# Kernel tuning notes

Hardware: AMD Instinct MI355X
Metric: run time of the kernel (lower is better)

## Reference

```python
import jax, jax.numpy as jnp
import numpy as np

B, NX, C, KX = 16, 8192, 128, 16  # batch, grid size, channels, retained positive modes


def setup_inputs() -> dict:
    key = jax.random.key(0)
    k1, k2, k3 = jax.random.split(key, 3)
    x = jax.random.normal(k1, (B, NX, C), dtype=jnp.float32)
    scale = 1.0 / (C ** 2)
    w_real = scale * jax.random.uniform(k2, (KX + 1, C, C), dtype=jnp.float32)
    w_imag = scale * jax.random.uniform(k3, (KX + 1, C, C), dtype=jnp.float32)
    return {"x": x, "w_real": w_real, "w_imag": w_imag}


def reference(x, w_real, w_imag):
    # x: (b, nx, c); weights: (kx+1, c, c) complex
    nx = x.shape[1]
    k1 = w_real.shape[0]  # kx + 1 retained frequencies
    w = w_real + 1j * w_imag
    fx = jnp.fft.rfft(x, axis=-2)  # (b, nx//2+1, c) complex
    # torch.matmul(weights, fx[:, :kx+1, :, None])[..., 0]:
    # out[b,k,i] = sum_j w[k,i,j] * fx[b,k,j]
    out_ft = jnp.einsum('kij,bkj->bki', w, fx[:, :k1, :])
    # zero-pad truncated spectrum back to full rfft length, then inverse
    pad = nx // 2 + 1 - k1
    out_full = jnp.pad(out_ft, ((0, 0), (0, pad), (0, 0)))
    return jnp.fft.irfft(out_full, n=nx, axis=-2)
```

## Files before the change

kernel.cpp:

```cpp
#include <hip/hip_runtime.h>
#include <math.h>

#define B_     16
#define NX_    8192
#define C_     128
#define K1_    17
#define NC_    64
#define NH_    4096

typedef float v2f __attribute__((ext_vector_type(2)));

#define GPART_F ((size_t)B_ * K1_ * 2 * NC_ * C_)

__global__ __launch_bounds__(256) void k_fwd(const float* __restrict__ x,
                                             float* __restrict__ ws) {
    __shared__ float smem[8960];

    float* gpart = ws;
    const int b = blockIdx.y;
    const int c = blockIdx.x;
    const int t = threadIdx.x;
    const int j2 = t & 63;
    const int h = t >> 6;
    const int i0 = c * 64;

    {
        float2* tg = (float2*)smem;
        for (int idx = t; idx < 64 * K1_; idx += 256) {
            int i = idx / K1_;
            int k = idx - i * K1_;
            int m = (k * (i0 + i)) & (NX_ - 1);
            float rev = (float)m * (1.0f / (float)NX_);
            tg[idx] = make_float2(__builtin_amdgcn_cosf(rev),
                                  __builtin_amdgcn_sinf(rev));
        }
    }
    __syncthreads();

    v2f gr[K1_], gs[K1_];
#pragma unroll
    for (int k = 0; k < K1_; ++k) { gr[k] = (v2f)(0.f); gs[k] = (v2f)(0.f); }

    const size_t xb = (size_t)b * NX_ * C_;
    const float2* tl = (const float2*)smem + (size_t)h * 16 * K1_;
#pragma unroll 4
    for (int s = 0; s < 16; ++s) {
        const int i = h * 16 + s;
        const int nlo = i0 + i;
        v2f xlo = *(const v2f*)(x + xb + (size_t)nlo * C_ + 2 * j2);
        v2f xhi = (v2f)(0.f);
        if (nlo > 0)
            xhi = *(const v2f*)(x + xb + (size_t)(NX_ - nlo) * C_ + 2 * j2);
        v2f xp = xlo + xhi;
        v2f xm = xlo - xhi;
        const float2* tr = tl + s * K1_;
#pragma unroll
        for (int k = 0; k < K1_; ++k) {
            float2 tt = tr[k];
            v2f cc = {tt.x, tt.x};
            v2f ss = {tt.y, tt.y};
            gr[k] = __builtin_elementwise_fma(xp, cc, gr[k]);
            gs[k] = __builtin_elementwise_fma(xm, ss, gs[k]);
        }
    }

    float2* red = (float2*)smem;
    __syncthreads();
    if (h >= 2) {
        float2* p = red + ((h - 2) * 64 + j2) * 35;
#pragma unroll
        for (int k = 0; k < K1_; ++k) {
            p[2 * k]     = make_float2(gr[k].x, gr[k].y);
            p[2 * k + 1] = make_float2(gs[k].x, gs[k].y);
        }
    }
    __syncthreads();
    if (h < 2) {
        const float2* p = red + (h * 64 + j2) * 35;
#pragma unroll
        for (int k = 0; k < K1_; ++k) {
            float2 a = p[2 * k], cc = p[2 * k + 1];
            gr[k].x += a.x;  gr[k].y += a.y;
            gs[k].x += cc.x; gs[k].y += cc.y;
        }
    }
    __syncthreads();
    if (h == 1) {
        float2* p = red + j2 * 35;
#pragma unroll
        for (int k = 0; k < K1_; ++k) {
            p[2 * k]     = make_float2(gr[k].x, gr[k].y);
            p[2 * k + 1] = make_float2(gs[k].x, gs[k].y);
        }
    }
    __syncthreads();
    if (h == 0) {
        const float2* p = red + j2 * 35;
        v2f x4 = (v2f)(0.f);
        if (c == 0)
            x4 = *(const v2f*)(x + xb + (size_t)NH_ * C_ + 2 * j2);
#pragma unroll
        for (int k = 0; k < K1_; ++k) {
            float2 a = p[2 * k], cc = p[2 * k + 1];
            gr[k].x += a.x;  gr[k].y += a.y;
            gs[k].x += cc.x; gs[k].y += cc.y;
            gr[k] += (k & 1) ? -x4 : x4;
            float* gpR = gpart + ((((size_t)b * K1_ + k) * 2 + 0) * NC_ + c) * C_;
            float* gpS = gpart + ((((size_t)b * K1_ + k) * 2 + 1) * NC_ + c) * C_;
            ((v2f*)gpR)[j2] = gr[k];
            ((v2f*)gpS)[j2] = gs[k];
        }
    }
}

__global__ __launch_bounds__(256) void k_mix(const float* __restrict__ wr_g,
                                             const float* __restrict__ wi_g,
                                             float* __restrict__ ws) {
    const int k = blockIdx.x;
    const int b = blockIdx.y;
    const int t = threadIdx.x;
    const int i = t & 127;
    const int h = t >> 7;

    const float* gpart = ws;
    float2* acoef = (float2*)(ws + GPART_F);

    __shared__ float grs[C_], gss[C_], tr_[C_], ti_[C_];

    const float* baseR = gpart + (((size_t)b * K1_ + k) * 2 + 0) * ((size_t)NC_ * C_);
    const float* baseS = gpart + (((size_t)b * K1_ + k) * 2 + 1) * ((size_t)NC_ * C_);
    float gr = 0.f, gs = 0.f;
#pragma unroll
    for (int s = 0; s < 32; ++s) {
        gr += baseR[(size_t)(h * 32 + s) * C_ + i];
        gs += baseS[(size_t)(h * 32 + s) * C_ + i];
    }
    if (h) { tr_[i] = gr; ti_[i] = gs; }
    __syncthreads();
    if (!h) { grs[i] = gr + tr_[i]; gss[i] = gs + ti_[i]; }
    __syncthreads();

    float hr = 0.f, hi = 0.f;
    const float* wrp = wr_g + ((size_t)k * C_ + i) * C_;
    const float* wip = wi_g + ((size_t)k * C_ + i) * C_;
#pragma unroll 8
    for (int jj = h * 64; jj < h * 64 + 64; ++jj) {
        float wr = wrp[jj], wi = wip[jj];
        float a = grs[jj], cc = gss[jj];
        hr = fmaf(wr, a, hr); hr = fmaf( wi, cc, hr);
        hi = fmaf(wi, a, hi); hi = fmaf(-wr, cc, hi);
    }
    __syncthreads();
    if (h) { tr_[i] = hr; ti_[i] = hi; }
    __syncthreads();
    if (!h) {
        hr += tr_[i]; hi += ti_[i];
        float cf = (k == 0 ? 1.0f : 2.0f) / (float)NX_;
        acoef[((size_t)b * K1_ + k) * C_ + i] = make_float2(cf * hr, -cf * hi);
    }
}

__global__ __launch_bounds__(256) void k_inv(float* __restrict__ out,
                                             const float* __restrict__ ws) {
    __shared__ float2 smem[64 * K1_];

    const float4* acoef4 = (const float4*)(ws + GPART_F);
    const int b = blockIdx.y;
    const int c = blockIdx.x;
    const int t = threadIdx.x;
    const int jp = t & 63;
    const int h = t >> 6;
    const int i0 = c * 64;

    for (int idx = t; idx < 64 * K1_; idx += 256) {
        int i = idx / K1_;
        int k = idx - i * K1_;
        int m = (k * (i0 + i)) & (NX_ - 1);
        float rev = (float)m * (1.0f / (float)NX_);
        smem[idx] = make_float2(__builtin_amdgcn_cosf(rev),
                                __builtin_amdgcn_sinf(rev));
    }

    v2f arP[K1_], aiP[K1_];
#pragma unroll
    for (int k = 0; k < K1_; ++k) {
        float4 a = acoef4[((size_t)b * K1_ + k) * (C_ / 2) + jp];
        arP[k] = (v2f){a.x, a.z};
        aiP[k] = (v2f){a.y, a.w};
    }
    __syncthreads();

    const size_t ob = (size_t)b * NX_ * C_;
    const float2* tl = smem + (size_t)h * 16 * K1_;
#pragma unroll 4
    for (int s = 0; s < 16; ++s) {
        const int nlo = i0 + h * 16 + s;
        const float2* tr = tl + s * K1_;
        v2f S1 = (v2f)(0.f), S2 = (v2f)(0.f);
#pragma unroll
        for (int k = 0; k < K1_; ++k) {
            float2 tt = tr[k];
            v2f cc = {tt.x, tt.x};
            v2f ss = {tt.y, tt.y};
            S1 = __builtin_elementwise_fma(arP[k], cc, S1);
            S2 = __builtin_elementwise_fma(aiP[k], ss, S2);
        }
        *(v2f*)(out + ob + (size_t)nlo * C_ + 2 * jp) = S1 + S2;
        if (nlo > 0)
            *(v2f*)(out + ob + (size_t)(NX_ - nlo) * C_ + 2 * jp) = S1 - S2;
    }

    if (c == 0 && h == 0) {
        v2f o = (v2f)(0.f);
#pragma unroll
        for (int k = 0; k < K1_; ++k) o += (k & 1) ? -arP[k] : arP[k];
        *(v2f*)(out + ob + (size_t)NH_ * C_ + 2 * jp) = o;
    }
}

extern "C" void kernel_launch(void* const* d_in, const int* in_sizes, int n_in,
                              void* d_out, int out_size, void* d_ws, size_t ws_size,
                              hipStream_t stream) {
    const float* x  = (const float*)d_in[0];
    const float* wr = (const float*)d_in[1];
    const float* wi = (const float*)d_in[2];
    float* out = (float*)d_out;
    float* ws  = (float*)d_ws;

    k_fwd<<<dim3(NC_, B_), 256, 0, stream>>>(x, ws);
    k_mix<<<dim3(K1_, B_), 256, 0, stream>>>(wr, wi, ws);
    k_inv<<<dim3(NC_, B_), 256, 0, stream>>>(out, ws);
}
```

Baseline: 53.63 us.

## Split forward DFT frequencies across half-waves with float4 loads; widen mix kernel

The forward kernel now has each thread load four channels as a float4 and handle half of the retained frequencies, 9 of 18 padded. This halves per-thread accumulator count and doubles the work done per memory load, and the Nyquist correction moves before the reduction. The mix kernel moves from 256 to 1024 threads per block, splitting both the partial-sum reduction and the weight contraction into more, shorter pieces for more parallelism. Costs are an extra padded frequency slot and more shared-memory reduction traffic.

```diff
diff --git a/kernel.cpp b/kernel.cpp
--- a/kernel.cpp
+++ b/kernel.cpp
@@ -5,156 +5,172 @@
 #define NX_    8192
 #define C_     128
 #define K1_    17
+#define KP_    18
 #define NC_    64
 #define NH_    4096
 
 typedef float v2f __attribute__((ext_vector_type(2)));
+typedef float v4f __attribute__((ext_vector_type(4)));
 
 #define GPART_F ((size_t)B_ * K1_ * 2 * NC_ * C_)
 
 __global__ __launch_bounds__(256) void k_fwd(const float* __restrict__ x,
                                              float* __restrict__ ws) {
-    __shared__ float smem[8960];
+    __shared__ v4f smem[2 * 64 * 19];
 
     float* gpart = ws;
     const int b = blockIdx.y;
     const int c = blockIdx.x;
     const int t = threadIdx.x;
-    const int j2 = t & 63;
-    const int h = t >> 6;
-    const int i0 = c * 64;
+    const int jq  = t & 31;
+    const int sub = (t >> 5) & 1;
+    const int w   = t >> 6;
+    const int i0  = c * 64;
 
     {
         float2* tg = (float2*)smem;
-        for (int idx = t; idx < 64 * K1_; idx += 256) {
-            int i = idx / K1_;
-            int k = idx - i * K1_;
-            int m = (k * (i0 + i)) & (NX_ - 1);
-            float rev = (float)m * (1.0f / (float)NX_);
-            tg[idx] = make_float2(__builtin_amdgcn_cosf(rev),
-                                  __builtin_amdgcn_sinf(rev));
-        }
-    }
-    __syncthreads();
-
-    v2f gr[K1_], gs[K1_];
-#pragma unroll
-    for (int k = 0; k < K1_; ++k) { gr[k] = (v2f)(0.f); gs[k] = (v2f)(0.f); }
+        for (int idx = t; idx < 64 * KP_; idx += 256) {
+            int i = idx / KP_;
+            int k = idx - i * KP_;
+            float2 v = make_float2(0.f, 0.f);
+            if (k < K1_) {
+                int m = (k * (i0 + i)) & (NX_ - 1);
+                float rev = (float)m * (1.0f / (float)NX_);
+                v = make_float2(__builtin_amdgcn_cosf(rev),
+                                __builtin_amdgcn_sinf(rev));
+            }
+            tg[idx] = v;
+        }
+    }
+    __syncthreads();
+
+    v4f gr[9], gs[9];
+#pragma unroll
+    for (int kk = 0; kk < 9; ++kk) { gr[kk] = (v4f)(0.f); gs[kk] = (v4f)(0.f); }
 
     const size_t xb = (size_t)b * NX_ * C_;
-    const float2* tl = (const float2*)smem + (size_t)h * 16 * K1_;
+    const int ibase = w * 16;
+    const float2* tp = (const float2*)smem + (size_t)ibase * KP_ + sub * 9;
+    const float* xlo_p = x + xb + (size_t)(i0 + ibase) * C_ + 4 * jq;
+    const float* xhi_p = x + xb + (size_t)(NX_ - (i0 + ibase)) * C_ + 4 * jq;
+
 #pragma unroll 4
     for (int s = 0; s < 16; ++s) {
-        const int i = h * 16 + s;
-        const int nlo = i0 + i;
-        v2f xlo = *(const v2f*)(x + xb + (size_t)nlo * C_ + 2 * j2);
-        v2f xhi = (v2f)(0.f);
+        const int nlo = i0 + ibase + s;
+        v4f xlo = *(const v4f*)(xlo_p + (size_t)s * C_);
+        v4f xhi = (v4f)(0.f);
         if (nlo > 0)
-            xhi = *(const v2f*)(x + xb + (size_t)(NX_ - nlo) * C_ + 2 * j2);
-        v2f xp = xlo + xhi;
-        v2f xm = xlo - xhi;
-        const float2* tr = tl + s * K1_;
-#pragma unroll
-        for (int k = 0; k < K1_; ++k) {
-            float2 tt = tr[k];
-            v2f cc = {tt.x, tt.x};
-            v2f ss = {tt.y, tt.y};
-            gr[k] = __builtin_elementwise_fma(xp, cc, gr[k]);
-            gs[k] = __builtin_elementwise_fma(xm, ss, gs[k]);
-        }
-    }
-
-    float2* red = (float2*)smem;
-    __syncthreads();
-    if (h >= 2) {
-        float2* p = red + ((h - 2) * 64 + j2) * 35;
-#pragma unroll
-        for (int k = 0; k < K1_; ++k) {
-            p[2 * k]     = make_float2(gr[k].x, gr[k].y);
-            p[2 * k + 1] = make_float2(gs[k].x, gs[k].y);
-        }
-    }
-    __syncthreads();
-    if (h < 2) {
-        const float2* p = red + (h * 64 + j2) * 35;
-#pragma unroll
-        for (int k = 0; k < K1_; ++k) {
-            float2 a = p[2 * k], cc = p[2 * k + 1];
-            gr[k].x += a.x;  gr[k].y += a.y;
-            gs[k].x += cc.x; gs[k].y += cc.y;
-        }
-    }
-    __syncthreads();
-    if (h == 1) {
-        float2* p = red + j2 * 35;
-#pragma unroll
-        for (int k = 0; k < K1_; ++k) {
-            p[2 * k]     = make_float2(gr[k].x, gr[k].y);
-            p[2 * k + 1] = make_float2(gs[k].x, gs[k].y);
-        }
-    }
-    __syncthreads();
-    if (h == 0) {
-        const float2* p = red + j2 * 35;
-        v2f x4 = (v2f)(0.f);
-        if (c == 0)
-            x4 = *(const v2f*)(x + xb + (size_t)NH_ * C_ + 2 * j2);
-#pragma unroll
-        for (int k = 0; k < K1_; ++k) {
-            float2 a = p[2 * k], cc = p[2 * k + 1];
-            gr[k].x += a.x;  gr[k].y += a.y;
-            gs[k].x += cc.x; gs[k].y += cc.y;
-            gr[k] += (k & 1) ? -x4 : x4;
-            float* gpR = gpart + ((((size_t)b * K1_ + k) * 2 + 0) * NC_ + c) * C_;
-            float* gpS = gpart + ((((size_t)b * K1_ + k) * 2 + 1) * NC_ + c) * C_;
-            ((v2f*)gpR)[j2] = gr[k];
-            ((v2f*)gpS)[j2] = gs[k];
-        }
-    }
-}
-
-__global__ __launch_bounds__(256) void k_mix(const float* __restrict__ wr_g,
-                                             const float* __restrict__ wi_g,
-                                             float* __restrict__ ws) {
+            xhi = *(const v4f*)(xhi_p - (size_t)s * C_);
+        v4f xp = xlo + xhi;
+        v4f xm = xlo - xhi;
+        const float2* tr = tp + (size_t)s * KP_;
+#pragma unroll
+        for (int kk = 0; kk < 9; ++kk) {
+            float2 tt = tr[kk];
+            gr[kk] = __builtin_elementwise_fma(xp, (v4f)(tt.x), gr[kk]);
+            gs[kk] = __builtin_elementwise_fma(xm, (v4f)(tt.y), gs[kk]);
+        }
+    }
+
+    if (c == 0 && w == 0) {
+        v4f x4 = *(const v4f*)(x + xb + (size_t)NH_ * C_ + 4 * jq);
+#pragma unroll
+        for (int kk = 0; kk < 9; ++kk) {
+            int k = sub * 9 + kk;
+            gr[kk] += (k & 1) ? -x4 : x4;
+        }
+    }
+
+    const int lid = t & 63;
+    __syncthreads();
+    if (w >= 2) {
+        v4f* p = smem + ((size_t)(w - 2) * 64 + lid) * 19;
+#pragma unroll
+        for (int kk = 0; kk < 9; ++kk) { p[2 * kk] = gr[kk]; p[2 * kk + 1] = gs[kk]; }
+    }
+    __syncthreads();
+    if (w < 2) {
+        const v4f* p = smem + ((size_t)w * 64 + lid) * 19;
+#pragma unroll
+        for (int kk = 0; kk < 9; ++kk) { gr[kk] += p[2 * kk]; gs[kk] += p[2 * kk + 1]; }
+    }
+    __syncthreads();
+    if (w == 1) {
+        v4f* p = smem + (size_t)lid * 19;
+#pragma unroll
+        for (int kk = 0; kk < 9; ++kk) { p[2 * kk] = gr[kk]; p[2 * kk + 1] = gs[kk]; }
+    }
+    __syncthreads();
+    if (w == 0) {
+        const v4f* p = smem + (size_t)lid * 19;
+#pragma unroll
+        for (int kk = 0; kk < 9; ++kk) {
+            gr[kk] += p[2 * kk];
+            gs[kk] += p[2 * kk + 1];
+            int k = sub * 9 + kk;
+            if (k < K1_) {
+                float* gpR = gpart + ((((size_t)b * K1_ + k) * 2 + 0) * NC_ + c) * C_ + 4 * jq;
+                float* gpS = gpart + ((((size_t)b * K1_ + k) * 2 + 1) * NC_ + c) * C_ + 4 * jq;
+                *(v4f*)gpR = gr[kk];
+                *(v4f*)gpS = gs[kk];
+            }
+        }
+    }
+}
+
+__global__ __launch_bounds__(1024) void k_mix(const float* __restrict__ wr_g,
+                                              const float* __restrict__ wi_g,
+                                              float* __restrict__ ws) {
     const int k = blockIdx.x;
     const int b = blockIdx.y;
     const int t = threadIdx.x;
-    const int i = t & 127;
-    const int h = t >> 7;
 
     const float* gpart = ws;
     float2* acoef = (float2*)(ws + GPART_F);
 
-    __shared__ float grs[C_], gss[C_], tr_[C_], ti_[C_];
-
-    const float* baseR = gpart + (((size_t)b * K1_ + k) * 2 + 0) * ((size_t)NC_ * C_);
-    const float* baseS = gpart + (((size_t)b * K1_ + k) * 2 + 1) * ((size_t)NC_ * C_);
-    float gr = 0.f, gs = 0.f;
-#pragma unroll
-    for (int s = 0; s < 32; ++s) {
-        gr += baseR[(size_t)(h * 32 + s) * C_ + i];
-        gs += baseS[(size_t)(h * 32 + s) * C_ + i];
-    }
-    if (h) { tr_[i] = gr; ti_[i] = gs; }
-    __syncthreads();
-    if (!h) { grs[i] = gr + tr_[i]; gss[i] = gs + ti_[i]; }
-    __syncthreads();
-
-    float hr = 0.f, hi = 0.f;
-    const float* wrp = wr_g + ((size_t)k * C_ + i) * C_;
-    const float* wip = wi_g + ((size_t)k * C_ + i) * C_;
-#pragma unroll 8
-    for (int jj = h * 64; jj < h * 64 + 64; ++jj) {
-        float wr = wrp[jj], wi = wip[jj];
-        float a = grs[jj], cc = gss[jj];
-        hr = fmaf(wr, a, hr); hr = fmaf( wi, cc, hr);
-        hi = fmaf(wi, a, hi); hi = fmaf(-wr, cc, hi);
-    }
-    __syncthreads();
-    if (h) { tr_[i] = hr; ti_[i] = hi; }
-    __syncthreads();
-    if (!h) {
-        hr += tr_[i]; hi += ti_[i];
+    __shared__ float part[8][C_];
+    __shared__ float gsum[2][C_];
+    __shared__ float hp[16][C_];
+
+    {
+        const int ch = t & 127, ri = (t >> 7) & 1, sh = t >> 8;
+        const float* base = gpart
+            + (((size_t)b * K1_ + k) * 2 + ri) * ((size_t)NC_ * C_) + ch;
+        float g = 0.f;
+#pragma unroll
+        for (int s = 0; s < 16; ++s) g += base[(size_t)(sh * 16 + s) * C_];
+        part[sh * 2 + ri][ch] = g;
+    }
+    __syncthreads();
+    if (t < 256) {
+        const int ch = t & 127, ri = t >> 7;
+        gsum[ri][ch] = part[ri][ch] + part[2 + ri][ch]
+                     + part[4 + ri][ch] + part[6 + ri][ch];
+    }
+    __syncthreads();
+
+    {
+        const int i = t & 127, q = t >> 7;
+        float hr = 0.f, hi = 0.f;
+        const float* wrp = wr_g + ((size_t)k * C_ + i) * C_;
+        const float* wip = wi_g + ((size_t)k * C_ + i) * C_;
+#pragma unroll
+        for (int jjj = 0; jjj < 16; ++jjj) {
+            int jj = q * 16 + jjj;
+            float wr = wrp[jj], wi = wip[jj];
+            float a = gsum[0][jj], cc = gsum[1][jj];
+            hr = fmaf(wr, a, hr); hr = fmaf( wi, cc, hr);
+            hi = fmaf(wi, a, hi); hi = fmaf(-wr, cc, hi);
+        }
+        hp[q * 2 + 0][i] = hr;
+        hp[q * 2 + 1][i] = hi;
+    }
+    __syncthreads();
+    if (t < 128) {
+        const int i = t;
+        float hr = 0.f, hi = 0.f;
+#pragma unroll
+        for (int q = 0; q < 8; ++q) { hr += hp[q * 2][i]; hi += hp[q * 2 + 1][i]; }
         float cf = (k == 0 ? 1.0f : 2.0f) / (float)NX_;
         acoef[((size_t)b * K1_ + k) * C_ + i] = make_float2(cf * hr, -cf * hi);
     }
@@ -228,6 +244,6 @@
     float* ws  = (float*)d_ws;
 
     k_fwd<<<dim3(NC_, B_), 256, 0, stream>>>(x, ws);
-    k_mix<<<dim3(K1_, B_), 256, 0, stream>>>(wr, wi, ws);
+    k_mix<<<dim3(K1_, B_), 1024, 0, stream>>>(wr, wi, ws);
     k_inv<<<dim3(NC_, B_), 256, 0, stream>>>(out, ws);
 }
```

Measured after the change: 52.90 us. No clear change (-1.3%).
